# Kernel optimization log

Measured on AMD Instinct MI355X. Metric: run time of the kernel, lower is better.

Reference implementation:

```python
import jax, jax.numpy as jnp
import numpy as np

B, T, C = 4, 2048, 1024
N_HEAD = 16
HEAD_DIM = C // N_HEAD
SCALE = 1.0 / np.sqrt(HEAD_DIM).astype(np.float32)


def setup_inputs() -> dict:
    key = jax.random.key(0)
    k1, k2, k3 = jax.random.split(key, 3)
    x = jax.random.normal(k1, (B, T, C), dtype=jnp.float32)
    # torch Linear weights: [out_features, in_features], scaled init
    w_qkv = jax.random.normal(k2, (3 * C, C), dtype=jnp.float32) * (1.0 / np.sqrt(C))
    w_out = jax.random.normal(k3, (C, C), dtype=jnp.float32) * (1.0 / np.sqrt(C))
    b_out = jnp.zeros((C,), dtype=jnp.float32)
    return {"x": x, "w_qkv": w_qkv, "w_out": w_out, "b_out": b_out}


def reference(x, w_qkv, w_out, b_out):
    Bsz, Tlen, Cdim = x.shape
    qkv = jnp.einsum('btc,oc->bto', x, w_qkv)  # [B,T,3C]
    q, k, v = jnp.split(qkv, 3, axis=-1)
    # [B,H,T,D]
    def heads(t):
        return t.reshape(Bsz, Tlen, N_HEAD, HEAD_DIM).transpose(0, 2, 1, 3)
    q, k, v = heads(q), heads(k), heads(v)
    att = jnp.einsum('bhqd,bhkd->bhqk', q, k) * SCALE  # [B,H,T,T]
    causal = jnp.tril(jnp.ones((Tlen, Tlen), dtype=bool))
    att = jnp.where(causal[None, None], att, -jnp.inf)
    att = jax.nn.softmax(att, axis=-1)
    out = jnp.einsum('bhqk,bhkd->bhqd', att, v)
    out = out.transpose(0, 2, 1, 3).reshape(Bsz, Tlen, Cdim)
    out = jnp.einsum('btc,oc->bto', out, w_out) + b_out
    return out
```

## Files before the change

kernel.cpp:

```cpp
#include <hip/hip_runtime.h>
#include <stdint.h>


typedef __attribute__((ext_vector_type(8))) short bf16x8;
typedef __attribute__((ext_vector_type(4))) float f32x4;

#define EXP2F(x) __builtin_amdgcn_exp2f(x)
#define SL2E 0.18033688011112042f
#define FIXED_M 15.0f

template <bool B> struct BoolC { static constexpr bool value = B; };

__device__ __forceinline__ short f2bf(float f) {
  union { float f; unsigned u; } c; c.f = f;
  unsigned u = c.u;
  unsigned r = (u + 0x7fffu + ((u >> 16) & 1u)) >> 16;
  return (short)(unsigned short)r;
}

__device__ __forceinline__ void softmax_pack(const f32x4* sc, bf16x8& pa0, bf16x8& pa1) {
  union U { int i[4]; bf16x8 v; };
  U u0, u1;
#pragma unroll
  for (int j = 0; j < 4; ++j) {
    float p0 = EXP2F(sc[j][0]);
    float p1 = EXP2F(sc[j][1]);
    float p2 = EXP2F(sc[j][2]);
    float p3 = EXP2F(sc[j][3]);
    int w0, w1;
    asm("v_cvt_pk_bf16_f32 %0, %1, %2" : "=v"(w0) : "v"(p0), "v"(p1));
    asm("v_cvt_pk_bf16_f32 %0, %1, %2" : "=v"(w1) : "v"(p2), "v"(p3));
    if (j < 2) { u0.i[j * 2] = w0; u0.i[j * 2 + 1] = w1; }
    else       { u1.i[(j - 2) * 2] = w0; u1.i[(j - 2) * 2 + 1] = w1; }
  }
  pa0 = u0.v;
  pa1 = u1.v;
}

__device__ __forceinline__ void llds16(const short* g, short* l) {
  __builtin_amdgcn_global_load_lds(
      (const __attribute__((address_space(1))) unsigned int*)g,
      (__attribute__((address_space(3))) unsigned int*)l, 16, 0, 0);
}

__global__ __launch_bounds__(256) void cast_all(
    const float* __restrict__ x, const float* __restrict__ wq,
    const float* __restrict__ wo, short* __restrict__ xb,
    short* __restrict__ wqb, short* __restrict__ wob) {
  const int b = blockIdx.x;
  const float* src;
  short* dst;
  int idx;
  if (b < 8192)        { src = x;  dst = xb;  idx = b * 256 + threadIdx.x; }
  else if (b < 11264)  { src = wq; dst = wqb; idx = (b - 8192) * 256 + threadIdx.x; }
  else                 { src = wo; dst = wob; idx = (b - 11264) * 256 + threadIdx.x; }
  float4 f = ((const float4*)src)[idx];
  short4 o;
  o.x = f2bf(f.x); o.y = f2bf(f.y); o.z = f2bf(f.z); o.w = f2bf(f.w);
  ((short4*)dst)[idx] = o;
}

__global__ __launch_bounds__(256) void gemm_qkv(
    const short* __restrict__ A, const short* __restrict__ Bw,
    short* __restrict__ Qo, short* __restrict__ Ko, short* __restrict__ Vt) {
  const int K = 1024;
  __shared__ short smem[17408];
  const int tid = threadIdx.x;
  const int lane = tid & 63;
  const int wave = tid >> 6;
  const int m0 = blockIdx.y * 128;
  const int n0 = blockIdx.x * 128;
  const int wm = (wave >> 1) * 64;
  const int wn = (wave & 1) * 64;
  const int mrow = lane & 15;
  const int kq = lane >> 4;

  f32x4 acc[4][4];
#pragma unroll
  for (int i = 0; i < 4; ++i)
#pragma unroll
    for (int j = 0; j < 4; ++j) acc[i][j] = (f32x4){0.f, 0.f, 0.f, 0.f};

  auto stage = [&](int it, int buf) {
#pragma unroll
    for (int call = 0; call < 2; ++call) {
      const int cb = call * 256 + wave * 64;
      const int c = cb + lane;
      const int row = c >> 2;
      const int scol = (c & 3) ^ ((row ^ (row >> 2)) & 3);
      llds16(A + (size_t)(m0 + row) * K + it * 32 + scol * 8,
             &smem[buf * 8192 + cb * 8]);
      llds16(Bw + (size_t)(n0 + row) * K + it * 32 + scol * 8,
             &smem[buf * 8192 + 4096 + cb * 8]);
    }
  };

  stage(0, 0);
  __syncthreads();

  for (int it = 0; it < 32; ++it) {
    const int buf = it & 1;
    if (it < 31) stage(it + 1, buf ^ 1);
    const short* lA = &smem[buf * 8192];
    const short* lB = &smem[buf * 8192 + 4096];
    bf16x8 af[4], bfr[4];
#pragma unroll
    for (int i = 0; i < 4; ++i) {
      const int row = wm + i * 16 + mrow;
      af[i] = *(const bf16x8*)&lA[row * 32 + (((kq ^ row ^ (row >> 2)) & 3) * 8)];
    }
#pragma unroll
    for (int j = 0; j < 4; ++j) {
      const int row = wn + j * 16 + mrow;
      bfr[j] = *(const bf16x8*)&lB[row * 32 + (((kq ^ row ^ (row >> 2)) & 3) * 8)];
    }
#pragma unroll
    for (int i = 0; i < 4; ++i)
#pragma unroll
      for (int j = 0; j < 4; ++j)
        acc[i][j] = __builtin_amdgcn_mfma_f32_16x16x32_bf16(af[i], bfr[j], acc[i][j], 0, 0, 0);
    __syncthreads();
  }

  const int b = m0 >> 11;
  if (n0 < 2048) {
    short* lC = smem;
#pragma unroll
    for (int i = 0; i < 4; ++i) {
      const int row = wm + i * 16 + kq * 4;
#pragma unroll
      for (int j = 0; j < 4; ++j) {
        const int col = wn + j * 16 + mrow;
        const float sc_ = (((n0 + col) >> 10) == 1) ? SL2E : 1.0f;
#pragma unroll
        for (int r = 0; r < 4; ++r)
          lC[(row + r) * 132 + col] = f2bf(acc[i][j][r] * sc_);
      }
    }
    __syncthreads();
#pragma unroll
    for (int call = 0; call < 8; ++call) {
      const int cc = call * 256 + tid;
      const int row = cc >> 4;
      const int t = (m0 + row) & 2047;
      const int o = n0 + (cc & 15) * 8;
      const int c = o & 1023;
      const int h = c >> 6;
      const int d = c & 63;
      short* dst = (o >> 10) == 0 ? Qo : Ko;
      bf16x8 val = *(const bf16x8*)&lC[row * 132 + (cc & 15) * 8];
      *(bf16x8*)(dst + ((size_t)(b * 16 + h) * 2048 + t) * 64 + d) = val;
    }
  } else {
    short* lCt = smem;
#pragma unroll
    for (int i = 0; i < 4; ++i) {
      const int row = wm + i * 16 + kq * 4;
#pragma unroll
      for (int j = 0; j < 4; ++j) {
        const int col = wn + j * 16 + mrow;
#pragma unroll
        for (int r = 0; r < 4; ++r)
          lCt[col * 136 + row + r] = f2bf(acc[i][j][r]);
      }
    }
    __syncthreads();
#pragma unroll
    for (int call = 0; call < 8; ++call) {
      const int cc = call * 256 + tid;
      const int col = cc >> 4;
      const int tg = cc & 15;
      const int o = n0 + col;
      const int d = o & 63;
      const int h = (o >> 6) & 15;
      const int t = (m0 & 2047) + tg * 8;
      bf16x8 val = *(const bf16x8*)&lCt[col * 136 + tg * 8];
      *(bf16x8*)(Vt + ((size_t)(b * 16 + h) * 64 + d) * 2048 + t) = val;
    }
  }
}

__global__ __launch_bounds__(256) void gemm_out(
    const short* __restrict__ A, const short* __restrict__ Bw,
    const float* __restrict__ bias, float* __restrict__ Out) {
  const int K = 1024;
  __shared__ short smem[16384];
  const int tid = threadIdx.x;
  const int lane = tid & 63;
  const int wave = tid >> 6;
  const int m0 = blockIdx.y * 128;
  const int n0 = blockIdx.x * 128;
  const int wm = (wave >> 1) * 64;
  const int wn = (wave & 1) * 64;
  const int mrow = lane & 15;
  const int kq = lane >> 4;

  f32x4 acc[4][4];
#pragma unroll
  for (int i = 0; i < 4; ++i)
#pragma unroll
    for (int j = 0; j < 4; ++j) acc[i][j] = (f32x4){0.f, 0.f, 0.f, 0.f};

  auto stage = [&](int it, int buf) {
#pragma unroll
    for (int call = 0; call < 2; ++call) {
      const int cb = call * 256 + wave * 64;
      const int c = cb + lane;
      const int row = c >> 2;
      const int scol = (c & 3) ^ ((row ^ (row >> 2)) & 3);
      llds16(A + (size_t)(m0 + row) * K + it * 32 + scol * 8,
             &smem[buf * 8192 + cb * 8]);
      llds16(Bw + (size_t)(n0 + row) * K + it * 32 + scol * 8,
             &smem[buf * 8192 + 4096 + cb * 8]);
    }
  };

  stage(0, 0);
  __syncthreads();

  for (int it = 0; it < 32; ++it) {
    const int buf = it & 1;
    if (it < 31) stage(it + 1, buf ^ 1);
    const short* lA = &smem[buf * 8192];
    const short* lB = &smem[buf * 8192 + 4096];
    bf16x8 af[4], bfr[4];
#pragma unroll
    for (int i = 0; i < 4; ++i) {
      const int row = wm + i * 16 + mrow;
      af[i] = *(const bf16x8*)&lA[row * 32 + (((kq ^ row ^ (row >> 2)) & 3) * 8)];
    }
#pragma unroll
    for (int j = 0; j < 4; ++j) {
      const int row = wn + j * 16 + mrow;
      bfr[j] = *(const bf16x8*)&lB[row * 32 + (((kq ^ row ^ (row >> 2)) & 3) * 8)];
    }
#pragma unroll
    for (int i = 0; i < 4; ++i)
#pragma unroll
      for (int j = 0; j < 4; ++j)
        acc[i][j] = __builtin_amdgcn_mfma_f32_16x16x32_bf16(af[i], bfr[j], acc[i][j], 0, 0, 0);
    __syncthreads();
  }

#pragma unroll
  for (int i = 0; i < 4; ++i) {
    const int m = m0 + wm + i * 16 + kq * 4;
#pragma unroll
    for (int j = 0; j < 4; ++j) {
      const int n = n0 + wn + j * 16 + mrow;
      const float bb = bias[n];
#pragma unroll
      for (int r = 0; r < 4; ++r)
        Out[(size_t)(m + r) * 1024 + n] = acc[i][j][r] + bb;
    }
  }
}

__global__ __launch_bounds__(256) void flash_attn(
    const short* __restrict__ Qg, const short* __restrict__ Kg,
    const short* __restrict__ Vtg, short* __restrict__ Og) {
  const int T = 2048;
  __shared__ short lK[2][64 * 64];
  __shared__ short lVt[2][64 * 64];
  const int tid = threadIdx.x;
  const int lane = tid & 63;
  const int wave = tid >> 6;
  const int bh = blockIdx.x;
  const int bx = blockIdx.y;
  const int mrow = lane & 15;
  const int kq = lane >> 4;
  const int swz = mrow & 7;
  const size_t base = (size_t)bh * T * 64;
  const size_t vbase = (size_t)bh * 64 * T;

  const int qt0 = bx;
  const int qt1 = 31 - bx;

  const bf16x8 ones = {0x3F80, 0x3F80, 0x3F80, 0x3F80, 0x3F80, 0x3F80, 0x3F80, 0x3F80};

  bf16x8 aq0_0, aq1_0, aq0_1, aq1_1;
  {
    const short* qp0 = Qg + base + (size_t)(qt0 * 64 + wave * 16 + mrow) * 64 + kq * 8;
    aq0_0 = *(const bf16x8*)qp0;
    aq1_0 = *(const bf16x8*)(qp0 + 32);
    const short* qp1 = Qg + base + (size_t)(qt1 * 64 + wave * 16 + mrow) * 64 + kq * 8;
    aq0_1 = *(const bf16x8*)qp1;
    aq1_1 = *(const bf16x8*)(qp1 + 32);
  }

  f32x4 acc0[4], acc1[4], lac0, lac1;
  lac0 = (f32x4){0.f, 0.f, 0.f, 0.f};
  lac1 = (f32x4){0.f, 0.f, 0.f, 0.f};
#pragma unroll
  for (int jd = 0; jd < 4; ++jd) {
    acc0[jd] = (f32x4){0.f, 0.f, 0.f, 0.f};
    acc1[jd] = (f32x4){0.f, 0.f, 0.f, 0.f};
  }

  auto stage = [&](int nt, int buf) {
#pragma unroll
    for (int call = 0; call < 2; ++call) {
      const int cb = call * 256 + wave * 64;
      const int c = cb + lane;
      const int row = c >> 3;
      const int scol = (c & 7) ^ (row & 7);
      const int grow = (row & 0x23) | ((row & 0x0C) << 1) | ((row & 0x10) >> 2);
      llds16(Kg + base + (size_t)(nt * 64 + grow) * 64 + scol * 8, &lK[buf][cb * 8]);
      llds16(Vtg + vbase + (size_t)row * T + nt * 64 + scol * 8, &lVt[buf][cb * 8]);
    }
  };

  stage(0, 0);
  __syncthreads();

  auto seg = [&](auto Aa, const short* K_, const short* Vt_, int kt) {
    constexpr bool ACT0 = decltype(Aa)::value;
    f32x4 sc0[4], sc1[4];
#pragma unroll
    for (int j = 0; j < 4; ++j) {
      const short* krow = &K_[(j * 16 + mrow) * 64];
      bf16x8 kb0 = *(const bf16x8*)&krow[(kq ^ swz) * 8];
      bf16x8 kb1 = *(const bf16x8*)&krow[((4 + kq) ^ swz) * 8];
      __builtin_amdgcn_s_setprio(1);
      f32x4 ss = (f32x4){-FIXED_M, -FIXED_M, -FIXED_M, -FIXED_M};
      ss = __builtin_amdgcn_mfma_f32_16x16x32_bf16(kb0, aq0_1, ss, 0, 0, 0);
      ss = __builtin_amdgcn_mfma_f32_16x16x32_bf16(kb1, aq1_1, ss, 0, 0, 0);
      sc1[j] = ss;
      if constexpr (ACT0) {
        f32x4 s2 = (f32x4){-FIXED_M, -FIXED_M, -FIXED_M, -FIXED_M};
        s2 = __builtin_amdgcn_mfma_f32_16x16x32_bf16(kb0, aq0_0, s2, 0, 0, 0);
        s2 = __builtin_amdgcn_mfma_f32_16x16x32_bf16(kb1, aq1_0, s2, 0, 0, 0);
        sc0[j] = s2;
      }
      __builtin_amdgcn_s_setprio(0);
    }

    if (kt == qt1) {
      const int qcol = qt1 * 64 + wave * 16 + mrow;
#pragma unroll
      for (int j = 0; j < 4; ++j) {
        const int keyb = kt * 64 + ((j & 2) << 4) + (kq << 3) + ((j & 1) << 2);
#pragma unroll
        for (int r = 0; r < 4; ++r)
          if (keyb + r > qcol) sc1[j][r] = -1e30f;
      }
    }
    if constexpr (ACT0) {
      if (kt == qt0) {
        const int qcol = qt0 * 64 + wave * 16 + mrow;
#pragma unroll
        for (int j = 0; j < 4; ++j) {
          const int keyb = kt * 64 + ((j & 2) << 4) + (kq << 3) + ((j & 1) << 2);
#pragma unroll
          for (int r = 0; r < 4; ++r)
            if (keyb + r > qcol) sc0[j][r] = -1e30f;
        }
      }
    }

    bf16x8 pa0_1, pa1_1, pa0_0, pa1_0;
    softmax_pack(sc1, pa0_1, pa1_1);
    lac1 = __builtin_amdgcn_mfma_f32_16x16x32_bf16(pa0_1, ones, lac1, 0, 0, 0);
    lac1 = __builtin_amdgcn_mfma_f32_16x16x32_bf16(pa1_1, ones, lac1, 0, 0, 0);
    if constexpr (ACT0) {
      softmax_pack(sc0, pa0_0, pa1_0);
      lac0 = __builtin_amdgcn_mfma_f32_16x16x32_bf16(pa0_0, ones, lac0, 0, 0, 0);
      lac0 = __builtin_amdgcn_mfma_f32_16x16x32_bf16(pa1_0, ones, lac0, 0, 0, 0);
    }

#pragma unroll
    for (int jd = 0; jd < 4; ++jd) {
      const short* vrow = &Vt_[(jd * 16 + mrow) * 64];
      bf16x8 vb0 = *(const bf16x8*)&vrow[(kq ^ swz) * 8];
      bf16x8 vb1 = *(const bf16x8*)&vrow[((4 + kq) ^ swz) * 8];
      __builtin_amdgcn_s_setprio(1);
      acc1[jd] = __builtin_amdgcn_mfma_f32_16x16x32_bf16(pa0_1, vb0, acc1[jd], 0, 0, 0);
      acc1[jd] = __builtin_amdgcn_mfma_f32_16x16x32_bf16(pa1_1, vb1, acc1[jd], 0, 0, 0);
      if constexpr (ACT0) {
        acc0[jd] = __builtin_amdgcn_mfma_f32_16x16x32_bf16(pa0_0, vb0, acc0[jd], 0, 0, 0);
        acc0[jd] = __builtin_amdgcn_mfma_f32_16x16x32_bf16(pa1_0, vb1, acc0[jd], 0, 0, 0);
      }
      __builtin_amdgcn_s_setprio(0);
    }
  };

  for (int kt = 0; kt <= qt1; ++kt) {
    const int bcur = kt & 1;
    if (kt < qt1) stage(kt + 1, bcur ^ 1);
    if (kt <= qt0) seg(BoolC<true>{}, lK[bcur], lVt[bcur], kt);
    else           seg(BoolC<false>{}, lK[bcur], lVt[bcur], kt);
    __syncthreads();
  }

  const int b = bh >> 4;
  const int h = bh & 15;
#pragma unroll
  for (int r = 0; r < 4; ++r) {
    const float inv0 = 1.0f / lac0[r];
    const int t0 = qt0 * 64 + wave * 16 + kq * 4 + r;
#pragma unroll
    for (int jd = 0; jd < 4; ++jd) {
      const int col = h * 64 + jd * 16 + mrow;
      Og[((size_t)b * 2048 + t0) * 1024 + col] = f2bf(acc0[jd][r] * inv0);
    }
    const float inv1 = 1.0f / lac1[r];
    const int t1 = qt1 * 64 + wave * 16 + kq * 4 + r;
#pragma unroll
    for (int jd = 0; jd < 4; ++jd) {
      const int col = h * 64 + jd * 16 + mrow;
      Og[((size_t)b * 2048 + t1) * 1024 + col] = f2bf(acc1[jd][r] * inv1);
    }
  }
}

extern "C" void kernel_launch(void* const* d_in, const int* in_sizes, int n_in,
                              void* d_out, int out_size, void* d_ws, size_t ws_size,
                              hipStream_t stream) {
  const float* x = (const float*)d_in[0];
  const float* w_qkv = (const float*)d_in[1];
  const float* w_out = (const float*)d_in[2];
  const float* b_out = (const float*)d_in[3];
  float* out = (float*)d_out;

  char* ws = (char*)d_ws;
  const size_t NX = 8192ull * 1024;
  const size_t NWQ = 3072ull * 1024;
  const size_t NWO = 1024ull * 1024;
  const size_t NQ = 64ull * 2048 * 64;
  size_t off = 0;
  short* xb    = (short*)(ws + off); off += NX * 2;
  short* wqkvb = (short*)(ws + off); off += NWQ * 2;
  short* woutb = (short*)(ws + off); off += NWO * 2;
  short* q     = (short*)(ws + off); off += NQ * 2;
  short* k     = (short*)(ws + off); off += NQ * 2;
  short* vt    = (short*)(ws + off); off += NQ * 2;
  short* attb  = (short*)(ws + off); off += NX * 2;
  if (off > ws_size) return;

  cast_all<<<12288, 256, 0, stream>>>(x, w_qkv, w_out, xb, wqkvb, woutb);
  gemm_qkv<<<dim3(24, 64), 256, 0, stream>>>(xb, wqkvb, q, k, vt);
  flash_attn<<<dim3(64, 16), 256, 0, stream>>>(q, k, vt, attb);
  gemm_out<<<dim3(8, 64), 256, 0, stream>>>(attb, woutb, b_out, out);
}
```

Measured before the change: 254.6 us.

## Restructure QKV GEMM to 256x128 tiles with 8 waves and phased ping-pong pipeline

The QKV projection GEMM now uses 512-thread blocks with 256x128 output tiles and a K-step of 64, so there are half as many blocks in M. The main loop is split into four barrier-separated phases. Each phase interleaves LDS fragment reads and the next tile's global-to-LDS loads with MFMA clusters under s_setprio and sched_barrier control. The goal is better reuse of the B tile and overlap of memory traffic with matrix math. In exchange it uses more LDS (96KB), adds more barriers per iteration, and changes register pressure and occupancy.

```diff
diff --git a/kernel.cpp b/kernel.cpp
--- a/kernel.cpp
+++ b/kernel.cpp
@@ -60,18 +60,18 @@
   ((short4*)dst)[idx] = o;
 }
 
-__global__ __launch_bounds__(256) void gemm_qkv(
+__global__ __launch_bounds__(512) void gemm_qkv(
     const short* __restrict__ A, const short* __restrict__ Bw,
     short* __restrict__ Qo, short* __restrict__ Ko, short* __restrict__ Vt) {
   const int K = 1024;
-  __shared__ short smem[17408];
+  __shared__ short smem[49152];
   const int tid = threadIdx.x;
   const int lane = tid & 63;
   const int wave = tid >> 6;
-  const int m0 = blockIdx.y * 128;
+  const int wr = wave >> 1;
+  const int wc = wave & 1;
+  const int m0 = blockIdx.y * 256;
   const int n0 = blockIdx.x * 128;
-  const int wm = (wave >> 1) * 64;
-  const int wn = (wave & 1) * 64;
   const int mrow = lane & 15;
   const int kq = lane >> 4;
 
@@ -81,100 +81,171 @@
 #pragma unroll
     for (int j = 0; j < 4; ++j) acc[i][j] = (f32x4){0.f, 0.f, 0.f, 0.f};
 
-  auto stage = [&](int it, int buf) {
-#pragma unroll
-    for (int call = 0; call < 2; ++call) {
-      const int cb = call * 256 + wave * 64;
-      const int c = cb + lane;
-      const int row = c >> 2;
-      const int scol = (c & 3) ^ ((row ^ (row >> 2)) & 3);
-      llds16(A + (size_t)(m0 + row) * K + it * 32 + scol * 8,
-             &smem[buf * 8192 + cb * 8]);
-      llds16(Bw + (size_t)(n0 + row) * K + it * 32 + scol * 8,
-             &smem[buf * 8192 + 4096 + cb * 8]);
-    }
-  };
-
-  stage(0, 0);
+  auto stageA = [&](int t, int buf, int ca) {
+    const int c = ca * 512 + tid;
+    const int row = c >> 3;
+    const int sc = (c & 7) ^ (row & 7);
+    llds16(A + (size_t)(m0 + row) * K + t * 64 + sc * 8,
+           &smem[buf * 24576 + c * 8]);
+  };
+  auto stageB = [&](int t, int buf, int cb) {
+    const int c = cb * 512 + tid;
+    const int row = c >> 3;
+    const int sc = (c & 7) ^ (row & 7);
+    llds16(Bw + (size_t)(n0 + row) * K + t * 64 + sc * 8,
+           &smem[buf * 24576 + 16384 + c * 8]);
+  };
+
+  auto rdA = [&](const short* lA, int i, int kk) -> bf16x8 {
+    const int row = wr * 64 + i * 16 + mrow;
+    const int ch = (kq + 4 * kk) ^ (row & 7);
+    return *(const bf16x8*)&lA[row * 64 + ch * 8];
+  };
+  auto rdB = [&](const short* lB, int j, int kk) -> bf16x8 {
+    const int row = wc * 64 + j * 16 + mrow;
+    const int ch = (kq + 4 * kk) ^ (row & 7);
+    return *(const bf16x8*)&lB[row * 64 + ch * 8];
+  };
+
+  stageA(0, 0, 0); stageA(0, 0, 1); stageA(0, 0, 2); stageA(0, 0, 3);
+  stageB(0, 0, 0); stageB(0, 0, 1);
+  asm volatile("s_waitcnt vmcnt(0)" ::: "memory");
   __syncthreads();
 
-  for (int it = 0; it < 32; ++it) {
-    const int buf = it & 1;
-    if (it < 31) stage(it + 1, buf ^ 1);
-    const short* lA = &smem[buf * 8192];
-    const short* lB = &smem[buf * 8192 + 4096];
-    bf16x8 af[4], bfr[4];
-#pragma unroll
-    for (int i = 0; i < 4; ++i) {
-      const int row = wm + i * 16 + mrow;
-      af[i] = *(const bf16x8*)&lA[row * 32 + (((kq ^ row ^ (row >> 2)) & 3) * 8)];
-    }
-#pragma unroll
-    for (int j = 0; j < 4; ++j) {
-      const int row = wn + j * 16 + mrow;
-      bfr[j] = *(const bf16x8*)&lB[row * 32 + (((kq ^ row ^ (row >> 2)) & 3) * 8)];
-    }
-#pragma unroll
-    for (int i = 0; i < 4; ++i)
-#pragma unroll
-      for (int j = 0; j < 4; ++j)
-        acc[i][j] = __builtin_amdgcn_mfma_f32_16x16x32_bf16(af[i], bfr[j], acc[i][j], 0, 0, 0);
-    __syncthreads();
-  }
+#define PHASE_TAIL()                                         \
+  __builtin_amdgcn_s_barrier();                              \
+  asm volatile("s_waitcnt lgkmcnt(0)" ::: "memory");         \
+  __builtin_amdgcn_sched_barrier(0);                         \
+  __builtin_amdgcn_s_setprio(1);
+
+#define PHASE_END()                                          \
+  __builtin_amdgcn_s_setprio(0);                             \
+  __builtin_amdgcn_sched_barrier(0);                         \
+  __builtin_amdgcn_s_barrier();
+
+  for (int t = 0; t < 16; ++t) {
+    const int buf = t & 1;
+    const int nb = buf ^ 1;
+    const short* lA = &smem[buf * 24576];
+    const short* lB = lA + 16384;
+    bf16x8 a0, a1, a2, a3, bf0, bf1, bf2, bf3;
+
+    a0 = rdA(lA, 0, 0); a1 = rdA(lA, 1, 0);
+    bf0 = rdB(lB, 0, 0); bf1 = rdB(lB, 1, 0);
+    bf2 = rdB(lB, 2, 0); bf3 = rdB(lB, 3, 0);
+    if (t < 15) { stageA(t + 1, nb, 0); stageA(t + 1, nb, 1); }
+    PHASE_TAIL();
+    acc[0][0] = __builtin_amdgcn_mfma_f32_16x16x32_bf16(a0, bf0, acc[0][0], 0, 0, 0);
+    acc[0][1] = __builtin_amdgcn_mfma_f32_16x16x32_bf16(a0, bf1, acc[0][1], 0, 0, 0);
+    acc[0][2] = __builtin_amdgcn_mfma_f32_16x16x32_bf16(a0, bf2, acc[0][2], 0, 0, 0);
+    acc[0][3] = __builtin_amdgcn_mfma_f32_16x16x32_bf16(a0, bf3, acc[0][3], 0, 0, 0);
+    acc[1][0] = __builtin_amdgcn_mfma_f32_16x16x32_bf16(a1, bf0, acc[1][0], 0, 0, 0);
+    acc[1][1] = __builtin_amdgcn_mfma_f32_16x16x32_bf16(a1, bf1, acc[1][1], 0, 0, 0);
+    acc[1][2] = __builtin_amdgcn_mfma_f32_16x16x32_bf16(a1, bf2, acc[1][2], 0, 0, 0);
+    acc[1][3] = __builtin_amdgcn_mfma_f32_16x16x32_bf16(a1, bf3, acc[1][3], 0, 0, 0);
+    PHASE_END();
+
+    a2 = rdA(lA, 2, 0); a3 = rdA(lA, 3, 0);
+    if (t < 15) { stageA(t + 1, nb, 2); stageA(t + 1, nb, 3); }
+    PHASE_TAIL();
+    acc[2][0] = __builtin_amdgcn_mfma_f32_16x16x32_bf16(a2, bf0, acc[2][0], 0, 0, 0);
+    acc[2][1] = __builtin_amdgcn_mfma_f32_16x16x32_bf16(a2, bf1, acc[2][1], 0, 0, 0);
+    acc[2][2] = __builtin_amdgcn_mfma_f32_16x16x32_bf16(a2, bf2, acc[2][2], 0, 0, 0);
+    acc[2][3] = __builtin_amdgcn_mfma_f32_16x16x32_bf16(a2, bf3, acc[2][3], 0, 0, 0);
+    acc[3][0] = __builtin_amdgcn_mfma_f32_16x16x32_bf16(a3, bf0, acc[3][0], 0, 0, 0);
+    acc[3][1] = __builtin_amdgcn_mfma_f32_16x16x32_bf16(a3, bf1, acc[3][1], 0, 0, 0);
+    acc[3][2] = __builtin_amdgcn_mfma_f32_16x16x32_bf16(a3, bf2, acc[3][2], 0, 0, 0);
+    acc[3][3] = __builtin_amdgcn_mfma_f32_16x16x32_bf16(a3, bf3, acc[3][3], 0, 0, 0);
+    PHASE_END();
+
+    a0 = rdA(lA, 0, 1); a1 = rdA(lA, 1, 1);
+    bf0 = rdB(lB, 0, 1); bf1 = rdB(lB, 1, 1);
+    bf2 = rdB(lB, 2, 1); bf3 = rdB(lB, 3, 1);
+    if (t < 15) { stageB(t + 1, nb, 0); stageB(t + 1, nb, 1); }
+    PHASE_TAIL();
+    acc[0][0] = __builtin_amdgcn_mfma_f32_16x16x32_bf16(a0, bf0, acc[0][0], 0, 0, 0);
+    acc[0][1] = __builtin_amdgcn_mfma_f32_16x16x32_bf16(a0, bf1, acc[0][1], 0, 0, 0);
+    acc[0][2] = __builtin_amdgcn_mfma_f32_16x16x32_bf16(a0, bf2, acc[0][2], 0, 0, 0);
+    acc[0][3] = __builtin_amdgcn_mfma_f32_16x16x32_bf16(a0, bf3, acc[0][3], 0, 0, 0);
+    acc[1][0] = __builtin_amdgcn_mfma_f32_16x16x32_bf16(a1, bf0, acc[1][0], 0, 0, 0);
+    acc[1][1] = __builtin_amdgcn_mfma_f32_16x16x32_bf16(a1, bf1, acc[1][1], 0, 0, 0);
+    acc[1][2] = __builtin_amdgcn_mfma_f32_16x16x32_bf16(a1, bf2, acc[1][2], 0, 0, 0);
+    acc[1][3] = __builtin_amdgcn_mfma_f32_16x16x32_bf16(a1, bf3, acc[1][3], 0, 0, 0);
+    PHASE_END();
+
+    a2 = rdA(lA, 2, 1); a3 = rdA(lA, 3, 1);
+    PHASE_TAIL();
+    acc[2][0] = __builtin_amdgcn_mfma_f32_16x16x32_bf16(a2, bf0, acc[2][0], 0, 0, 0);
+    acc[2][1] = __builtin_amdgcn_mfma_f32_16x16x32_bf16(a2, bf1, acc[2][1], 0, 0, 0);
+    acc[2][2] = __builtin_amdgcn_mfma_f32_16x16x32_bf16(a2, bf2, acc[2][2], 0, 0, 0);
+    acc[2][3] = __builtin_amdgcn_mfma_f32_16x16x32_bf16(a2, bf3, acc[2][3], 0, 0, 0);
+    acc[3][0] = __builtin_amdgcn_mfma_f32_16x16x32_bf16(a3, bf0, acc[3][0], 0, 0, 0);
+    acc[3][1] = __builtin_amdgcn_mfma_f32_16x16x32_bf16(a3, bf1, acc[3][1], 0, 0, 0);
+    acc[3][2] = __builtin_amdgcn_mfma_f32_16x16x32_bf16(a3, bf2, acc[3][2], 0, 0, 0);
+    acc[3][3] = __builtin_amdgcn_mfma_f32_16x16x32_bf16(a3, bf3, acc[3][3], 0, 0, 0);
+    __builtin_amdgcn_s_setprio(0);
+    __builtin_amdgcn_sched_barrier(0);
+    if (t < 15) asm volatile("s_waitcnt vmcnt(0)" ::: "memory");
+    __builtin_amdgcn_s_barrier();
+  }
+#undef PHASE_TAIL
+#undef PHASE_END
+
+  __syncthreads();
 
   const int b = m0 >> 11;
   if (n0 < 2048) {
+    const float sc_ = ((n0 >> 10) == 1) ? SL2E : 1.0f;
     short* lC = smem;
 #pragma unroll
     for (int i = 0; i < 4; ++i) {
-      const int row = wm + i * 16 + kq * 4;
+      const int rl = wr * 64 + i * 16 + kq * 4;
 #pragma unroll
       for (int j = 0; j < 4; ++j) {
-        const int col = wn + j * 16 + mrow;
-        const float sc_ = (((n0 + col) >> 10) == 1) ? SL2E : 1.0f;
+        const int col = wc * 64 + j * 16 + mrow;
 #pragma unroll
         for (int r = 0; r < 4; ++r)
-          lC[(row + r) * 132 + col] = f2bf(acc[i][j][r] * sc_);
+          lC[(rl + r) * 132 + col] = f2bf(acc[i][j][r] * sc_);
       }
     }
     __syncthreads();
+    short* dst = (n0 >> 10) == 0 ? Qo : Ko;
 #pragma unroll
     for (int call = 0; call < 8; ++call) {
-      const int cc = call * 256 + tid;
+      const int cc = call * 512 + tid;
       const int row = cc >> 4;
-      const int t = (m0 + row) & 2047;
-      const int o = n0 + (cc & 15) * 8;
-      const int c = o & 1023;
+      const int ch = cc & 15;
+      const int t = (m0 & 2047) + row;
+      const int c = (n0 + ch * 8) & 1023;
       const int h = c >> 6;
       const int d = c & 63;
-      short* dst = (o >> 10) == 0 ? Qo : Ko;
-      bf16x8 val = *(const bf16x8*)&lC[row * 132 + (cc & 15) * 8];
+      bf16x8 val = *(const bf16x8*)&lC[row * 132 + ch * 8];
       *(bf16x8*)(dst + ((size_t)(b * 16 + h) * 2048 + t) * 64 + d) = val;
     }
   } else {
     short* lCt = smem;
 #pragma unroll
     for (int i = 0; i < 4; ++i) {
-      const int row = wm + i * 16 + kq * 4;
+      const int rl = wr * 64 + i * 16 + kq * 4;
 #pragma unroll
       for (int j = 0; j < 4; ++j) {
-        const int col = wn + j * 16 + mrow;
+        const int col = wc * 64 + j * 16 + mrow;
 #pragma unroll
         for (int r = 0; r < 4; ++r)
-          lCt[col * 136 + row + r] = f2bf(acc[i][j][r]);
+          lCt[col * 264 + rl + r] = f2bf(acc[i][j][r]);
       }
     }
     __syncthreads();
 #pragma unroll
     for (int call = 0; call < 8; ++call) {
-      const int cc = call * 256 + tid;
-      const int col = cc >> 4;
-      const int tg = cc & 15;
+      const int cc = call * 512 + tid;
+      const int col = cc >> 5;
+      const int tg = cc & 31;
       const int o = n0 + col;
       const int d = o & 63;
       const int h = (o >> 6) & 15;
       const int t = (m0 & 2047) + tg * 8;
-      bf16x8 val = *(const bf16x8*)&lCt[col * 136 + tg * 8];
+      bf16x8 val = *(const bf16x8*)&lCt[col * 264 + tg * 8];
       *(bf16x8*)(Vt + ((size_t)(b * 16 + h) * 64 + d) * 2048 + t) = val;
     }
   }
@@ -438,7 +509,7 @@
   if (off > ws_size) return;
 
   cast_all<<<12288, 256, 0, stream>>>(x, w_qkv, w_out, xb, wqkvb, woutb);
-  gemm_qkv<<<dim3(24, 64), 256, 0, stream>>>(xb, wqkvb, q, k, vt);
+  gemm_qkv<<<dim3(24, 32), 512, 0, stream>>>(xb, wqkvb, q, k, vt);
   flash_attn<<<dim3(64, 16), 256, 0, stream>>>(q, k, vt, attb);
   gemm_out<<<dim3(8, 64), 256, 0, stream>>>(attb, woutb, b_out, out);
 }
```

After: 248.5 us. 2.4% less time.
